# Kernel optimization log

Hardware: AMD Instinct MI355X
Metric: run time of the kernel (lower is better)

The kernel has to match this reference:

```python
import jax, jax.numpy as jnp
import numpy as np

B, T, D = 32, 1024, 1024
N, L = 256, 768
H = 16
TE = 2048


def layernorm(x, g, b, eps=1e-5):
    m = jnp.mean(x, axis=-1, keepdims=True)
    v = jnp.var(x, axis=-1, keepdims=True)
    return (x - m) * jax.lax.rsqrt(v + eps) * g + b


def setup_inputs() -> dict:
    key = jax.random.key(0)
    ks = jax.random.split(key, 16)
    s = 0.02
    return {
        "x": jax.random.normal(ks[0], (B, T, D), jnp.float32),
        "xf": jax.random.normal(ks[1], (B, N, L), jnp.float32),
        "emb": jax.random.normal(ks[2], (B, TE), jnp.float32),
        "src_mask": jnp.ones((B, T, 1), jnp.float32),
        "cond_type": jax.random.randint(ks[3], (B, 1, 1), 0, 100),
        # LayerNorm params
        "ln_x_g": jnp.ones((D,), jnp.float32), "ln_x_b": jnp.zeros((D,), jnp.float32),
        "ln_t_g": jnp.ones((L,), jnp.float32), "ln_t_b": jnp.zeros((L,), jnp.float32),
        # Q/K/V projections
        "Wq": jax.random.normal(ks[4], (D, D), jnp.float32) * s, "bq": jnp.zeros((D,), jnp.float32),
        "Wk": jax.random.normal(ks[5], (L, D), jnp.float32) * s, "bk": jnp.zeros((D,), jnp.float32),
        "Wv": jax.random.normal(ks[6], (L, D), jnp.float32) * s, "bv": jnp.zeros((D,), jnp.float32),
        # StylizationBlock: SiLU -> Linear(TE, 2D); LayerNorm(D); SiLU -> Linear(D, D)
        "We": jax.random.normal(ks[7], (TE, 2 * D), jnp.float32) * s, "be": jnp.zeros((2 * D,), jnp.float32),
        "ln_y_g": jnp.ones((D,), jnp.float32), "ln_y_b": jnp.zeros((D,), jnp.float32),
        "Wo": jax.random.normal(ks[8], (D, D), jnp.float32) * s, "bo": jnp.zeros((D,), jnp.float32),
    }


def reference(x, xf, emb, src_mask, cond_type,
              ln_x_g, ln_x_b, ln_t_g, ln_t_b,
              Wq, bq, Wk, bk, Wv, bv,
              We, be, ln_y_g, ln_y_b, Wo, bo):
    Bh, Th, Dh = x.shape
    Nn = xf.shape[1]
    head = Dh // H

    # text condition gate: (B,1,1), constant per batch element
    tcond = (cond_type % 10 > 0).astype(x.dtype).reshape(Bh, 1, 1)

    q = (layernorm(x, ln_x_g, ln_x_b) @ Wq + bq).reshape(Bh, Th, H, head)
    xf_n = layernorm(xf, ln_t_g, ln_t_b)
    k = (xf_n @ Wk + bk).reshape(Bh, Nn, H, head)

    # B,T,N,H scores (note: no 1/sqrt(d) scaling, as in the original)
    att = jnp.einsum('bthd,bnhd->btnh', q, k)
    att = att + (1.0 - tcond.reshape(Bh, 1, 1, 1)) * -1000000.0
    att = jax.nn.softmax(att, axis=2)

    v = ((xf_n @ Wv + bv) * tcond).reshape(Bh, Nn, H, head)
    y = jnp.einsum('btnh,bnhd->bthd', att, v).reshape(Bh, Th, Dh)

    # StylizationBlock (dropout inactive in eval)
    emb_out = jax.nn.silu(emb) @ We + be            # B, 2D
    scale, shift = jnp.split(emb_out, 2, axis=-1)   # B, D each
    h = layernorm(y, ln_y_g, ln_y_b) * (1.0 + scale[:, None, :]) + shift[:, None, :]
    h = jax.nn.silu(h) @ Wo + bo
    return x + h
```

## Files before the change

kernel.cpp:

```cpp
#include <hip/hip_runtime.h>
#include <hip/hip_bf16.h>

#define DEV __device__ __forceinline__

typedef __attribute__((ext_vector_type(8))) short bf16x8;
typedef __attribute__((ext_vector_type(4))) float f32x4;
typedef __attribute__((ext_vector_type(8))) unsigned short u16x8;

DEV unsigned short f2bf(float f){
  unsigned int b = __float_as_uint(f);
  return (unsigned short)((b + 0x7fffu + ((b >> 16) & 1u)) >> 16);
}
DEV float bf2f(unsigned short u){ return __uint_as_float(((unsigned int)u)<<16); }

DEV float silu_f(float v){ return v / (1.f + __expf(-v)); }

DEV void gl_lds16(const void* g, void* l){
  __builtin_amdgcn_global_load_lds((const __attribute__((address_space(1))) void*)g,
                                   (__attribute__((address_space(3))) void*)l, 16, 0, 0);
}

DEV void wtile(const float* W, unsigned short* Wt, int K, int N, int nt, int kt, int tid,
               float (*tile)[33])
{
  int n0 = nt<<5, k0 = kt<<5;
  int tx = tid & 31, ty = tid >> 5;
  #pragma unroll
  for (int i=0;i<4;i++)
    tile[ty + i*8][tx] = W[(size_t)(k0 + ty + i*8)*N + n0 + tx];
  __syncthreads();
  #pragma unroll
  for (int i=0;i<4;i++)
    Wt[(size_t)(n0 + ty + i*8)*K + k0 + tx] = f2bf(tile[tx][ty + i*8]);
}

__global__ __launch_bounds__(256) void prep_ln(
    const float* __restrict__ x, const float* __restrict__ xf,
    const float* __restrict__ gx, const float* __restrict__ bx_,
    const float* __restrict__ gt, const float* __restrict__ bt,
    unsigned short* __restrict__ ox, unsigned short* __restrict__ ot,
    const float* __restrict__ Wq, const float* __restrict__ Wk,
    const float* __restrict__ Wv, const float* __restrict__ Wo,
    const float* __restrict__ bk, const float* __restrict__ bv,
    unsigned short* __restrict__ wqt, unsigned short* __restrict__ wkvt,
    unsigned short* __restrict__ wot, float* __restrict__ bkv)
{
  int row = blockIdx.x, t = threadIdx.x;
  if (row >= 40960){
    __shared__ float tile[32][33];
    int id = row - 40960;
    if (id < 8){
      int i = id*256 + t;
      bkv[i] = (i < 1024) ? bk[i] : bv[i-1024];
      return;
    }
    id -= 8;
    if (id < 1024){ wtile(Wq, wqt, 1024, 1024, id & 31, id >> 5, t, tile); return; }
    id -= 1024;
    if (id < 768){ wtile(Wk, wkvt, 768, 1024, id & 31, id >> 5, t, tile); return; }
    id -= 768;
    if (id < 768){ wtile(Wv, wkvt + (size_t)1024*768, 768, 1024, id & 31, id >> 5, t, tile); return; }
    id -= 768;
    wtile(Wo, wot, 1024, 1024, id & 31, id >> 5, t, tile);
    return;
  }
  const float* src; const float* g; const float* bb; unsigned short* out;
  int D, nvec;
  if (row < 32768){ src = x + (size_t)row*1024; g = gx; bb = bx_; out = ox + (size_t)row*1024; D = 1024; nvec = 256; }
  else { int r2 = row - 32768; src = xf + (size_t)r2*768; g = gt; bb = bt; out = ot + (size_t)r2*768; D = 768; nvec = 192; }
  float4 v = make_float4(0.f,0.f,0.f,0.f);
  if (t < nvec) v = ((const float4*)src)[t];
  float s  = v.x+v.y+v.z+v.w;
  float s2 = v.x*v.x+v.y*v.y+v.z*v.z+v.w*v.w;
  #pragma unroll
  for (int o=32;o;o>>=1){ s += __shfl_down(s,o,64); s2 += __shfl_down(s2,o,64); }
  __shared__ float red[8];
  if ((t&63)==0){ red[t>>6]=s; red[4+(t>>6)]=s2; }
  __syncthreads();
  float fs  = red[0]+red[1]+red[2]+red[3];
  float fs2 = red[4]+red[5]+red[6]+red[7];
  float mean = fs / (float)D;
  float var  = fmaxf(fs2/(float)D - mean*mean, 0.f);
  float rstd = rsqrtf(var + 1e-5f);
  if (t < nvec){
    float4 gv = ((const float4*)g)[t];
    float4 bv4 = ((const float4*)bb)[t];
    ushort4 o4;
    o4.x = f2bf((v.x-mean)*rstd*gv.x + bv4.x);
    o4.y = f2bf((v.y-mean)*rstd*gv.y + bv4.y);
    o4.z = f2bf((v.z-mean)*rstd*gv.z + bv4.z);
    o4.w = f2bf((v.w-mean)*rstd*gv.w + bv4.w);
    *(ushort4*)(out + t*4) = o4;
  }
}

template<int EPI>
__global__ __launch_bounds__(256,2) void gemm128(
  const unsigned char* __restrict__ A, const unsigned char* __restrict__ Wt,
  const float* __restrict__ bias, void* __restrict__ Cout,
  const float* __restrict__ Xadd, unsigned char* __restrict__ vt,
  int M, int N, int K, int gxshift)
{
  __shared__ __align__(16) unsigned char lds[65536];
  const int nwg = gridDim.x;
  const int chunk = nwg >> 3;
  const int wg = blockIdx.x;
  const int lg = (wg & 7) * chunk + (wg >> 3);
  const int bx = lg & ((1<<gxshift)-1);
  const int by = lg >> gxshift;
  const int tid = threadIdx.x, w = tid>>6, lane = tid&63;
  const int l15 = lane&15, lq = lane>>4;
  const int m0 = by<<7, n0 = bx<<7;
  const size_t K2 = (size_t)K<<1;
  const int KT = K>>6;
  const int wr = (w>>1)&1, wc = w&1;
  const int srow = lane>>3;
  const int scb  = (lane&7)<<4;

  f32x4 acc[4][4];
  f32x4 zero = {0.f,0.f,0.f,0.f};
  #pragma unroll
  for (int i=0;i<4;i++)
    #pragma unroll
    for (int j=0;j<4;j++) acc[i][j] = zero;

  auto stage = [&](int buf, int kt){
    unsigned char* ldsA = lds + buf*32768;
    const size_t kb = (size_t)kt<<7;
    #pragma unroll
    for (int inst=0; inst<4; ++inst){
      int base = w*1024 + inst*4096;
      int row  = (base>>7) + srow;
      int cs   = scb ^ ((row&7)<<4);
      gl_lds16(A  + (size_t)(m0+row)*K2 + kb + cs, ldsA + base);
      gl_lds16(Wt + (size_t)(n0+row)*K2 + kb + cs, ldsA + 16384 + base);
    }
  };

  stage(0, 0);
  __syncthreads();
  for (int kt=0; kt<KT; ++kt){
    if (kt+1 < KT) stage((kt+1)&1, kt+1);
    const unsigned char* ldsA = lds + (kt&1)*32768;
    const unsigned char* ldsB = ldsA + 16384;
    bf16x8 af[2][4], bfr[2][4];
    #pragma unroll
    for (int i=0;i<4;i++){
      int r = wr*64 + i*16 + l15;
      int rb = r<<7, sw = (r&7)<<4;
      af[0][i] = *(const bf16x8*)(ldsA + rb + ((lq*16) ^ sw));
      af[1][i] = *(const bf16x8*)(ldsA + rb + ((64 + lq*16) ^ sw));
    }
    #pragma unroll
    for (int j=0;j<4;j++){
      int r = wc*64 + j*16 + l15;
      int rb = r<<7, sw = (r&7)<<4;
      bfr[0][j] = *(const bf16x8*)(ldsB + rb + ((lq*16) ^ sw));
      bfr[1][j] = *(const bf16x8*)(ldsB + rb + ((64 + lq*16) ^ sw));
    }
    #pragma unroll
    for (int kc=0;kc<2;kc++)
      #pragma unroll
      for (int i=0;i<4;i++)
        #pragma unroll
        for (int j=0;j<4;j++)
          acc[i][j] = __builtin_amdgcn_mfma_f32_16x16x32_bf16(af[kc][i], bfr[kc][j], acc[i][j], 0,0,0);
    __syncthreads();
  }
  #pragma unroll
  for (int j=0;j<4;j++){
    int n = n0 + wc*64 + j*16 + l15;
    float bvs = bias[n];
    #pragma unroll
    for (int i=0;i<4;i++){
      int mb = m0 + wr*64 + i*16 + lq*4;
      #pragma unroll
      for (int r=0;r<4;r++){
        int m = mb + r;
        float val = acc[i][j][r] + bvs;
        if (EPI==0){
          ((unsigned short*)Cout)[(size_t)m*N + n] = f2bf(val);
        } else if (EPI==1){
          size_t idx = (size_t)m*N + n;
          ((float*)Cout)[idx] = Xadd[idx] + val;
        } else {
          if (n0 < 1024){
            ((unsigned short*)Cout)[(size_t)m*1024 + n] = f2bf(val);
          } else {
            int d  = (n-1024)&63;
            int hh = (n-1024)>>6;
            int bb_ = m>>8, nk = m&255;
            *(unsigned short*)(vt + ((size_t)(bb_*16+hh)<<15) + d*512
                + (((nk>>3)<<4) ^ ((d&7)<<4)) + ((nk&7)<<1)) = f2bf(val);
          }
        }
      }
    }
  }
}

__global__ __launch_bounds__(256,2) void attn64(
  const unsigned char* __restrict__ qg, const unsigned char* __restrict__ kg,
  int kstride, const unsigned char* __restrict__ vtg, const int* __restrict__ cond,
  unsigned short* __restrict__ yout)
{
  __shared__ __align__(16) unsigned char lds[73728];
  const int wg = blockIdx.x;
  const int lg = (wg & 7) * 1024 + (wg >> 3);
  const int t0 = (lg & 15) * 64;
  const int h  = (lg >> 4) & 15;
  const int b  = lg >> 8;
  const int tid = threadIdx.x, w = tid>>6, lane = tid&63;
  const int l15 = lane&15, lq = lane>>4;

  const unsigned char* kbase = kg + (size_t)b*256*kstride + (size_t)h*128;
  const unsigned char* vtb   = vtg + (size_t)(b*16+h)*32768;
  #pragma unroll
  for (int i=0;i<8;i++){
    int base = (w*8+i)*1024;
    int n  = (base>>7) + (lane>>3);
    int cb = (lane&7)<<4;
    gl_lds16(kbase + (size_t)n*kstride + (cb ^ ((n&7)<<4)), lds + base);
    gl_lds16(vtb + base + lane*16, lds + 32768 + base);
  }
  const unsigned char* qbase = qg + (size_t)(b*1024 + t0)*2048 + h*128;
  #pragma unroll
  for (int i=0;i<2;i++){
    int row = i*32 + (tid>>3);
    int cs  = ((tid&7)<<4) ^ ((row&7)<<4);
    gl_lds16(qbase + (size_t)row*2048 + cs, lds + 65536 + i*4096 + w*1024);
  }
  __syncthreads();

  const int qr = w*16 + l15;
  const int qsw = (qr&7)<<4;
  bf16x8 aq0 = *(const bf16x8*)(lds + 65536 + qr*128 + ((lq*16) ^ qsw));
  bf16x8 aq1 = *(const bf16x8*)(lds + 65536 + qr*128 + ((64 + lq*16) ^ qsw));

  f32x4 zero = {0.f,0.f,0.f,0.f};
  f32x4 s[16];
  #pragma unroll
  for (int nt=0;nt<16;nt++) s[nt] = zero;
  #pragma unroll
  for (int nt=0;nt<16;nt++){
    int n = nt*16 + l15;
    int rb = n<<7, sw = (n&7)<<4;
    bf16x8 kb0 = *(const bf16x8*)(lds + rb + ((lq*16) ^ sw));
    bf16x8 kb1 = *(const bf16x8*)(lds + rb + ((64 + lq*16) ^ sw));
    s[nt] = __builtin_amdgcn_mfma_f32_16x16x32_bf16(aq0, kb0, s[nt], 0,0,0);
    s[nt] = __builtin_amdgcn_mfma_f32_16x16x32_bf16(aq1, kb1, s[nt], 0,0,0);
  }
  #pragma unroll
  for (int r=0;r<4;r++){
    float m = s[0][r];
    #pragma unroll
    for (int nt=1;nt<16;nt++) m = fmaxf(m, s[nt][r]);
    m = fmaxf(m, __shfl_xor(m,1,64));
    m = fmaxf(m, __shfl_xor(m,2,64));
    m = fmaxf(m, __shfl_xor(m,4,64));
    m = fmaxf(m, __shfl_xor(m,8,64));
    float sum = 0.f;
    #pragma unroll
    for (int nt=0;nt<16;nt++){ float p = __expf(s[nt][r]-m); s[nt][r]=p; sum+=p; }
    sum += __shfl_xor(sum,1,64);
    sum += __shfl_xor(sum,2,64);
    sum += __shfl_xor(sum,4,64);
    sum += __shfl_xor(sum,8,64);
    float inv = 1.f/sum;
    #pragma unroll
    for (int nt=0;nt<16;nt++) s[nt][r] *= inv;
  }
  __syncthreads();
  #pragma unroll
  for (int nt=0;nt<16;nt++){
    int n = nt*16 + l15;
    int nb = (n>>3)<<4, nr = (n&7)<<1;
    #pragma unroll
    for (int r=0;r<4;r++){
      int tl = w*16 + lq*4 + r;
      *(unsigned short*)(lds + tl*512 + ((nb ^ ((tl&7)<<4)) | nr)) = f2bf(s[nt][r]);
    }
  }
  __syncthreads();
  f32x4 yv[4];
  #pragma unroll
  for (int dt=0;dt<4;dt++) yv[dt] = zero;
  const int tl = w*16 + l15;
  const int swp = (tl&7)<<4;
  #pragma unroll
  for (int kc=0;kc<8;kc++){
    bf16x8 pa = *(const bf16x8*)(lds + tl*512 + ((kc*64 + lq*16) ^ swp));
    #pragma unroll
    for (int dt=0;dt<4;dt++){
      int d = dt*16 + l15;
      bf16x8 vbv = *(const bf16x8*)(lds + 32768 + d*512 + ((kc*64 + lq*16) ^ ((d&7)<<4)));
      yv[dt] = __builtin_amdgcn_mfma_f32_16x16x32_bf16(pa, vbv, yv[dt], 0,0,0);
    }
  }
  float tc = (cond[b] % 10 > 0) ? 1.f : 0.f;
  #pragma unroll
  for (int dt=0;dt<4;dt++){
    #pragma unroll
    for (int r=0;r<4;r++){
      int tt = t0 + w*16 + lq*4 + r;
      yout[(size_t)(b*1024 + tt)*1024 + h*64 + dt*16 + l15] = f2bf(yv[dt][r]*tc);
    }
  }
}

__global__ __launch_bounds__(256) void embgemm(const float* __restrict__ emb,
    const float* __restrict__ We, float* __restrict__ epart)
{
  __shared__ float a[32][128];
  int cb = blockIdx.x, ks = blockIdx.y, tid = threadIdx.x;
  int k0 = ks<<7;
  #pragma unroll
  for (int it=0; it<4; ++it){
    int fi = it*256 + tid;
    int r = fi>>5, c4 = (fi&31)<<2;
    float4 vv = *(const float4*)(emb + (size_t)r*2048 + k0 + c4);
    vv.x = silu_f(vv.x); vv.y = silu_f(vv.y); vv.z = silu_f(vv.z); vv.w = silu_f(vv.w);
    *(float4*)&a[r][c4] = vv;
  }
  __syncthreads();
  int c0 = (cb<<8) + tid;
  float acc[32];
  #pragma unroll
  for (int r=0;r<32;r++) acc[r]=0.f;
  for (int kk=0;kk<128;kk++){
    float wv = We[(size_t)(k0+kk)*2048 + c0];
    #pragma unroll
    for (int r=0;r<32;r++) acc[r] += a[r][kk]*wv;
  }
  #pragma unroll
  for (int r=0;r<32;r++) epart[(size_t)(ks*32 + r)*2048 + c0] = acc[r];
}

__global__ __launch_bounds__(256) void embred(const float* __restrict__ epart,
    const float* __restrict__ be, float* __restrict__ eo)
{
  int idx = blockIdx.x*256 + threadIdx.x;
  float s = be[idx & 2047];
  #pragma unroll
  for (int ks=0;ks<16;ks++) s += epart[(size_t)ks*65536 + idx];
  eo[idx] = s;
}

__global__ __launch_bounds__(256) void styl(const unsigned short* __restrict__ y,
    const float* __restrict__ g, const float* __restrict__ bt,
    const float* __restrict__ eo, unsigned short* __restrict__ hout)
{
  int row = blockIdx.x, t = threadIdx.x, b = row>>10;
  ushort4 yv4 = ((const ushort4*)(y + (size_t)row*1024))[t];
  float in[4] = {bf2f(yv4.x), bf2f(yv4.y), bf2f(yv4.z), bf2f(yv4.w)};
  float s  = in[0]+in[1]+in[2]+in[3];
  float s2 = in[0]*in[0]+in[1]*in[1]+in[2]*in[2]+in[3]*in[3];
  #pragma unroll
  for (int o=32;o;o>>=1){ s += __shfl_down(s,o,64); s2 += __shfl_down(s2,o,64); }
  __shared__ float red[8];
  if ((t&63)==0){ red[t>>6]=s; red[4+(t>>6)]=s2; }
  __syncthreads();
  float fs  = red[0]+red[1]+red[2]+red[3];
  float fs2 = red[4]+red[5]+red[6]+red[7];
  float mean = fs*(1.f/1024.f);
  float var  = fmaxf(fs2*(1.f/1024.f) - mean*mean, 0.f);
  float rstd = rsqrtf(var + 1e-5f);
  float4 gv = ((const float4*)g)[t];
  float4 bv = ((const float4*)bt)[t];
  float4 sc = ((const float4*)(eo + (size_t)b*2048))[t];
  float4 sh = ((const float4*)(eo + (size_t)b*2048 + 1024))[t];
  float gg[4]  = {gv.x,gv.y,gv.z,gv.w};
  float bb[4]  = {bv.x,bv.y,bv.z,bv.w};
  float scs[4] = {sc.x,sc.y,sc.z,sc.w};
  float shs[4] = {sh.x,sh.y,sh.z,sh.w};
  unsigned short oo[4];
  #pragma unroll
  for (int c=0;c<4;c++){
    float hv = (in[c]-mean)*rstd*gg[c] + bb[c];
    hv = hv*(1.f+scs[c]) + shs[c];
    oo[c] = f2bf(silu_f(hv));
  }
  ushort4 o4; o4.x=oo[0]; o4.y=oo[1]; o4.z=oo[2]; o4.w=oo[3];
  *(ushort4*)(hout + (size_t)row*1024 + t*4) = o4;
}

extern "C" void kernel_launch(void* const* d_in, const int* in_sizes, int n_in,
                              void* d_out, int out_size, void* d_ws, size_t ws_size,
                              hipStream_t stream) {
  const float* x      = (const float*)d_in[0];
  const float* xf     = (const float*)d_in[1];
  const float* emb    = (const float*)d_in[2];
  const int*   cond   = (const int*)d_in[4];
  const float* ln_x_g = (const float*)d_in[5];
  const float* ln_x_b = (const float*)d_in[6];
  const float* ln_t_g = (const float*)d_in[7];
  const float* ln_t_b = (const float*)d_in[8];
  const float* Wq     = (const float*)d_in[9];
  const float* bq     = (const float*)d_in[10];
  const float* Wk     = (const float*)d_in[11];
  const float* bk     = (const float*)d_in[12];
  const float* Wv     = (const float*)d_in[13];
  const float* bv     = (const float*)d_in[14];
  const float* We     = (const float*)d_in[15];
  const float* be     = (const float*)d_in[16];
  const float* ln_y_g = (const float*)d_in[17];
  const float* ln_y_b = (const float*)d_in[18];
  const float* Wo     = (const float*)d_in[19];
  const float* bo     = (const float*)d_in[20];
  float* out = (float*)d_out;

  unsigned char* ws = (unsigned char*)d_ws;
  size_t off = 0;
  auto take = [&](size_t n){ unsigned char* p = ws + off; off += (n + 255) & ~(size_t)255; return p; };
  unsigned char* r1   = take(67108864);
  unsigned char* qb   = take(67108864);
  unsigned char* xfn  = take(12582912);
  unsigned char* kb   = take(16777216);
  unsigned char* vtb  = take(16777216);
  unsigned char* wqt  = take(2097152);
  unsigned char* wkvt = take(3145728);
  unsigned char* wot  = take(2097152);
  unsigned char* eo   = take(262144);
  unsigned char* bkv  = take(8192);
  float* epart = (float*)r1;

  dim3 blk(256);
  prep_ln<<<44552, blk, 0, stream>>>(x, xf, ln_x_g, ln_x_b, ln_t_g, ln_t_b,
      (unsigned short*)r1, (unsigned short*)xfn,
      Wq, Wk, Wv, Wo, bk, bv,
      (unsigned short*)wqt, (unsigned short*)wkvt, (unsigned short*)wot, (float*)bkv);
  gemm128<0><<<2048, blk, 0, stream>>>(r1, wqt, bq, qb, nullptr, nullptr, 32768, 1024, 1024, 3);
  gemm128<2><<<1024, blk, 0, stream>>>(xfn, wkvt, (const float*)bkv, kb, nullptr, vtb, 8192, 2048, 768, 4);
  embgemm<<<dim3(8,16), blk, 0, stream>>>(emb, We, epart);
  embred<<<256, blk, 0, stream>>>(epart, be, (float*)eo);
  attn64<<<8192, blk, 0, stream>>>(qb, kb, 2048, vtb, cond, (unsigned short*)qb);
  styl<<<32768, blk, 0, stream>>>((const unsigned short*)qb, ln_y_g, ln_y_b, (const float*)eo, (unsigned short*)r1);
  gemm128<1><<<2048, blk, 0, stream>>>(r1, wot, bo, out, x, nullptr, 32768, 1024, 1024, 3);
}
```

Before: 462.4 us.

## Merge small kernels into grouped launches and skip attention for masked batches

Folds the embedding GEMM into the prep kernel's extra blocks. One launch now runs the Q projection, the KV projection and the embedding reduction as a grouped grid, so there are fewer launches and the Q and KV GEMMs can run concurrently. The attention kernel exits early and writes zeros for batch elements whose text condition is off, since V is zeroed there. The prep kernel now reserves a larger shared buffer for every block, and the skip helps only for batches where the condition is off.

```diff
diff --git a/kernel.cpp b/kernel.cpp
--- a/kernel.cpp
+++ b/kernel.cpp
@@ -43,11 +43,13 @@
     const float* __restrict__ Wv, const float* __restrict__ Wo,
     const float* __restrict__ bk, const float* __restrict__ bv,
     unsigned short* __restrict__ wqt, unsigned short* __restrict__ wkvt,
-    unsigned short* __restrict__ wot, float* __restrict__ bkv)
-{
+    unsigned short* __restrict__ wot, float* __restrict__ bkv,
+    const float* __restrict__ emb, const float* __restrict__ We,
+    float* __restrict__ epart)
+{
+  __shared__ float shbuf[4096];
   int row = blockIdx.x, t = threadIdx.x;
   if (row >= 40960){
-    __shared__ float tile[32][33];
     int id = row - 40960;
     if (id < 8){
       int i = id*256 + t;
@@ -55,13 +57,41 @@
       return;
     }
     id -= 8;
-    if (id < 1024){ wtile(Wq, wqt, 1024, 1024, id & 31, id >> 5, t, tile); return; }
-    id -= 1024;
-    if (id < 768){ wtile(Wk, wkvt, 768, 1024, id & 31, id >> 5, t, tile); return; }
-    id -= 768;
-    if (id < 768){ wtile(Wv, wkvt + (size_t)1024*768, 768, 1024, id & 31, id >> 5, t, tile); return; }
-    id -= 768;
-    wtile(Wo, wot, 1024, 1024, id & 31, id >> 5, t, tile);
+    if (id < 3584){
+      float (*tile)[33] = (float(*)[33])shbuf;
+      if (id < 1024){ wtile(Wq, wqt, 1024, 1024, id & 31, id >> 5, t, tile); return; }
+      id -= 1024;
+      if (id < 768){ wtile(Wk, wkvt, 768, 1024, id & 31, id >> 5, t, tile); return; }
+      id -= 768;
+      if (id < 768){ wtile(Wv, wkvt + (size_t)1024*768, 768, 1024, id & 31, id >> 5, t, tile); return; }
+      id -= 768;
+      wtile(Wo, wot, 1024, 1024, id & 31, id >> 5, t, tile);
+      return;
+    }
+    id -= 3584;
+    float (*a)[128] = (float(*)[128])shbuf;
+    int cb = id & 7, ks = id >> 3;
+    int k0 = ks << 7;
+    #pragma unroll
+    for (int it=0; it<4; ++it){
+      int fi = it*256 + t;
+      int r = fi>>5, c4 = (fi&31)<<2;
+      float4 vv = *(const float4*)(emb + (size_t)r*2048 + k0 + c4);
+      vv.x = silu_f(vv.x); vv.y = silu_f(vv.y); vv.z = silu_f(vv.z); vv.w = silu_f(vv.w);
+      *(float4*)&a[r][c4] = vv;
+    }
+    __syncthreads();
+    int c0 = (cb<<8) + t;
+    float accv[32];
+    #pragma unroll
+    for (int r=0;r<32;r++) accv[r]=0.f;
+    for (int kk=0;kk<128;kk++){
+      float wv = We[(size_t)(k0+kk)*2048 + c0];
+      #pragma unroll
+      for (int r=0;r<32;r++) accv[r] += a[r][kk]*wv;
+    }
+    #pragma unroll
+    for (int r=0;r<32;r++) epart[(size_t)(ks*32 + r)*2048 + c0] = accv[r];
     return;
   }
   const float* src; const float* g; const float* bb; unsigned short* out;
@@ -74,11 +104,10 @@
   float s2 = v.x*v.x+v.y*v.y+v.z*v.z+v.w*v.w;
   #pragma unroll
   for (int o=32;o;o>>=1){ s += __shfl_down(s,o,64); s2 += __shfl_down(s2,o,64); }
-  __shared__ float red[8];
-  if ((t&63)==0){ red[t>>6]=s; red[4+(t>>6)]=s2; }
-  __syncthreads();
-  float fs  = red[0]+red[1]+red[2]+red[3];
-  float fs2 = red[4]+red[5]+red[6]+red[7];
+  if ((t&63)==0){ shbuf[t>>6]=s; shbuf[4+(t>>6)]=s2; }
+  __syncthreads();
+  float fs  = shbuf[0]+shbuf[1]+shbuf[2]+shbuf[3];
+  float fs2 = shbuf[4]+shbuf[5]+shbuf[6]+shbuf[7];
   float mean = fs / (float)D;
   float var  = fmaxf(fs2/(float)D - mean*mean, 0.f);
   float rstd = rsqrtf(var + 1e-5f);
@@ -95,19 +124,12 @@
 }
 
 template<int EPI>
-__global__ __launch_bounds__(256,2) void gemm128(
+DEV void gemm_body(
   const unsigned char* __restrict__ A, const unsigned char* __restrict__ Wt,
   const float* __restrict__ bias, void* __restrict__ Cout,
   const float* __restrict__ Xadd, unsigned char* __restrict__ vt,
-  int M, int N, int K, int gxshift)
-{
-  __shared__ __align__(16) unsigned char lds[65536];
-  const int nwg = gridDim.x;
-  const int chunk = nwg >> 3;
-  const int wg = blockIdx.x;
-  const int lg = (wg & 7) * chunk + (wg >> 3);
-  const int bx = lg & ((1<<gxshift)-1);
-  const int by = lg >> gxshift;
+  int M, int N, int K, int bx, int by, unsigned char* lds)
+{
   const int tid = threadIdx.x, w = tid>>6, lane = tid&63;
   const int l15 = lane&15, lq = lane>>4;
   const int m0 = by<<7, n0 = bx<<7;
@@ -199,6 +221,37 @@
   }
 }
 
+__global__ __launch_bounds__(256,2) void qkv(
+  const unsigned char* __restrict__ xln, const unsigned char* __restrict__ wqt,
+  const float* __restrict__ bq, unsigned char* __restrict__ qb,
+  const unsigned char* __restrict__ xfn, const unsigned char* __restrict__ wkvt,
+  const float* __restrict__ bkv, unsigned char* __restrict__ kb,
+  unsigned char* __restrict__ vtb,
+  const float* __restrict__ epart, const float* __restrict__ be,
+  float* __restrict__ eo)
+{
+  __shared__ __align__(16) unsigned char lds[65536];
+  int wg = blockIdx.x;
+  if (wg < 2048){
+    int lg = (wg & 7) * 256 + (wg >> 3);
+    gemm_body<0>(xln, wqt, bq, qb, nullptr, nullptr, 32768, 1024, 1024, lg & 7, lg >> 3, lds);
+  } else if (wg < 3072){
+    int w2 = wg - 2048;
+    int lg = (w2 & 7) * 128 + (w2 >> 3);
+    gemm_body<2>(xfn, wkvt, bkv, kb, nullptr, vtb, 8192, 2048, 768, lg & 15, lg >> 4, lds);
+  } else {
+    int idx0 = (wg - 3072) * 2048 + threadIdx.x;
+    #pragma unroll
+    for (int e=0;e<8;e++){
+      int idx = idx0 + e*256;
+      float s = be[idx & 2047];
+      #pragma unroll
+      for (int ks=0;ks<16;ks++) s += epart[(size_t)ks*65536 + idx];
+      eo[idx] = s;
+    }
+  }
+}
+
 __global__ __launch_bounds__(256,2) void attn64(
   const unsigned char* __restrict__ qg, const unsigned char* __restrict__ kg,
   int kstride, const unsigned char* __restrict__ vtg, const int* __restrict__ cond,
@@ -213,6 +266,15 @@
   const int tid = threadIdx.x, w = tid>>6, lane = tid&63;
   const int l15 = lane&15, lq = lane>>4;
 
+  if (cond[b] % 10 == 0){
+    int row = t0 + (tid>>2);
+    unsigned short* dst = yout + (size_t)(b*1024 + row)*1024 + h*64 + (tid&3)*16;
+    u16x8 z = {0,0,0,0,0,0,0,0};
+    *(u16x8*)dst = z;
+    *(u16x8*)(dst + 8) = z;
+    return;
+  }
+
   const unsigned char* kbase = kg + (size_t)b*256*kstride + (size_t)h*128;
   const unsigned char* vtb   = vtg + (size_t)(b*16+h)*32768;
   #pragma unroll
@@ -297,53 +359,14 @@
       yv[dt] = __builtin_amdgcn_mfma_f32_16x16x32_bf16(pa, vbv, yv[dt], 0,0,0);
     }
   }
-  float tc = (cond[b] % 10 > 0) ? 1.f : 0.f;
   #pragma unroll
   for (int dt=0;dt<4;dt++){
     #pragma unroll
     for (int r=0;r<4;r++){
       int tt = t0 + w*16 + lq*4 + r;
-      yout[(size_t)(b*1024 + tt)*1024 + h*64 + dt*16 + l15] = f2bf(yv[dt][r]*tc);
-    }
-  }
-}
-
-__global__ __launch_bounds__(256) void embgemm(const float* __restrict__ emb,
-    const float* __restrict__ We, float* __restrict__ epart)
-{
-  __shared__ float a[32][128];
-  int cb = blockIdx.x, ks = blockIdx.y, tid = threadIdx.x;
-  int k0 = ks<<7;
-  #pragma unroll
-  for (int it=0; it<4; ++it){
-    int fi = it*256 + tid;
-    int r = fi>>5, c4 = (fi&31)<<2;
-    float4 vv = *(const float4*)(emb + (size_t)r*2048 + k0 + c4);
-    vv.x = silu_f(vv.x); vv.y = silu_f(vv.y); vv.z = silu_f(vv.z); vv.w = silu_f(vv.w);
-    *(float4*)&a[r][c4] = vv;
-  }
-  __syncthreads();
-  int c0 = (cb<<8) + tid;
-  float acc[32];
-  #pragma unroll
-  for (int r=0;r<32;r++) acc[r]=0.f;
-  for (int kk=0;kk<128;kk++){
-    float wv = We[(size_t)(k0+kk)*2048 + c0];
-    #pragma unroll
-    for (int r=0;r<32;r++) acc[r] += a[r][kk]*wv;
-  }
-  #pragma unroll
-  for (int r=0;r<32;r++) epart[(size_t)(ks*32 + r)*2048 + c0] = acc[r];
-}
-
-__global__ __launch_bounds__(256) void embred(const float* __restrict__ epart,
-    const float* __restrict__ be, float* __restrict__ eo)
-{
-  int idx = blockIdx.x*256 + threadIdx.x;
-  float s = be[idx & 2047];
-  #pragma unroll
-  for (int ks=0;ks<16;ks++) s += epart[(size_t)ks*65536 + idx];
-  eo[idx] = s;
+      yout[(size_t)(b*1024 + tt)*1024 + h*64 + dt*16 + l15] = f2bf(yv[dt][r]);
+    }
+  }
 }
 
 __global__ __launch_bounds__(256) void styl(const unsigned short* __restrict__ y,
@@ -382,6 +405,17 @@
   }
   ushort4 o4; o4.x=oo[0]; o4.y=oo[1]; o4.z=oo[2]; o4.w=oo[3];
   *(ushort4*)(hout + (size_t)row*1024 + t*4) = o4;
+}
+
+__global__ __launch_bounds__(256,2) void gemmO(
+  const unsigned char* __restrict__ A, const unsigned char* __restrict__ Wt,
+  const float* __restrict__ bias, float* __restrict__ Cout,
+  const float* __restrict__ Xadd)
+{
+  __shared__ __align__(16) unsigned char lds[65536];
+  int wg = blockIdx.x;
+  int lg = (wg & 7) * 256 + (wg >> 3);
+  gemm_body<1>(A, Wt, bias, Cout, Xadd, nullptr, 32768, 1024, 1024, lg & 7, lg >> 3, lds);
 }
 
 extern "C" void kernel_launch(void* const* d_in, const int* in_sizes, int n_in,
@@ -412,28 +446,28 @@
   unsigned char* ws = (unsigned char*)d_ws;
   size_t off = 0;
   auto take = [&](size_t n){ unsigned char* p = ws + off; off += (n + 255) & ~(size_t)255; return p; };
-  unsigned char* r1   = take(67108864);
-  unsigned char* qb   = take(67108864);
-  unsigned char* xfn  = take(12582912);
-  unsigned char* kb   = take(16777216);
-  unsigned char* vtb  = take(16777216);
-  unsigned char* wqt  = take(2097152);
-  unsigned char* wkvt = take(3145728);
-  unsigned char* wot  = take(2097152);
-  unsigned char* eo   = take(262144);
-  unsigned char* bkv  = take(8192);
-  float* epart = (float*)r1;
+  unsigned char* r1    = take(67108864);
+  unsigned char* qb    = take(67108864);
+  unsigned char* xfn   = take(12582912);
+  unsigned char* kb    = take(16777216);
+  unsigned char* vtb   = take(16777216);
+  unsigned char* wqt   = take(2097152);
+  unsigned char* wkvt  = take(3145728);
+  unsigned char* wot   = take(2097152);
+  unsigned char* eo    = take(262144);
+  unsigned char* bkv   = take(8192);
+  unsigned char* epart = take(4194304);
 
   dim3 blk(256);
-  prep_ln<<<44552, blk, 0, stream>>>(x, xf, ln_x_g, ln_x_b, ln_t_g, ln_t_b,
+  prep_ln<<<44680, blk, 0, stream>>>(x, xf, ln_x_g, ln_x_b, ln_t_g, ln_t_b,
       (unsigned short*)r1, (unsigned short*)xfn,
       Wq, Wk, Wv, Wo, bk, bv,
-      (unsigned short*)wqt, (unsigned short*)wkvt, (unsigned short*)wot, (float*)bkv);
-  gemm128<0><<<2048, blk, 0, stream>>>(r1, wqt, bq, qb, nullptr, nullptr, 32768, 1024, 1024, 3);
-  gemm128<2><<<1024, blk, 0, stream>>>(xfn, wkvt, (const float*)bkv, kb, nullptr, vtb, 8192, 2048, 768, 4);
-  embgemm<<<dim3(8,16), blk, 0, stream>>>(emb, We, epart);
-  embred<<<256, blk, 0, stream>>>(epart, be, (float*)eo);
+      (unsigned short*)wqt, (unsigned short*)wkvt, (unsigned short*)wot, (float*)bkv,
+      emb, We, (float*)epart);
+  qkv<<<3104, blk, 0, stream>>>(r1, wqt, bq, qb,
+      xfn, wkvt, (const float*)bkv, kb, vtb,
+      (const float*)epart, be, (float*)eo);
   attn64<<<8192, blk, 0, stream>>>(qb, kb, 2048, vtb, cond, (unsigned short*)qb);
   styl<<<32768, blk, 0, stream>>>((const unsigned short*)qb, ln_y_g, ln_y_b, (const float*)eo, (unsigned short*)r1);
-  gemm128<1><<<2048, blk, 0, stream>>>(r1, wot, bo, out, x, nullptr, 32768, 1024, 1024, 3);
-}
+  gemmO<<<2048, blk, 0, stream>>>(r1, wot, bo, out, x);
+}
```

Measured after the change: 477.9 us. +3.4%, slower.
